# Kernel tuning notes

Hardware: AMD Instinct MI355X
Metric: run time of the kernel (lower is better)

Reference implementation:

```python
import jax, jax.numpy as jnp
import numpy as np

K = 1024
DIM = 64
BETA = 0.25  # commitment coefficient


def setup_inputs() -> dict:
    key = jax.random.key(0)
    k1, k2 = jax.random.split(key)
    x = jax.random.normal(k1, (32, 64, 64, 64), dtype=jnp.float32)  # [b, d, h, w]
    lookup_table = jax.random.normal(k2, (K, DIM), dtype=jnp.float32)  # [k, dim]
    return {"x": x, "lookup_table": lookup_table}


def reference(x, lookup_table):
    b, d, h, w = x.shape
    sg = jax.lax.stop_gradient
    # flatten to tokens: [b*h*w, dim]
    xf = jnp.transpose(x, (0, 2, 3, 1)).reshape(-1, d)
    # squared Euclidean distances (argmin-equivalent to cdist): [N, K]
    d2 = (jnp.sum(xf * xf, axis=1, keepdims=True)
          - 2.0 * (xf @ lookup_table.T)
          + jnp.sum(lookup_table * lookup_table, axis=1))
    q_x = jnp.argmin(d2, axis=1)  # [N]
    # gather codes and restore [b, d, h, w]
    x_e = jnp.transpose(lookup_table[q_x].reshape(b, h, w, d), (0, 3, 1, 2))
    # codebook + commitment loss (EMA update disabled in source)
    codebook_loss = jnp.mean((sg(x) - x_e) ** 2) + BETA * jnp.mean((x - sg(x_e)) ** 2)
    out = x + sg(x - x_e)
    return out, q_x.reshape(b, h, w), codebook_loss
```

## Files before the change

kernel.cpp:

```cpp
#include <hip/hip_runtime.h>

#define QX_OFF    8388608
#define LOSS_OFF  8519680
#define MARGIN_V  0.02f

typedef __attribute__((ext_vector_type(8))) short bf16x8;
typedef __attribute__((ext_vector_type(4))) float f32x4;
typedef unsigned long long u64;
typedef unsigned int u32;

static __device__ __forceinline__ unsigned short rne_bf16(float f) {
    unsigned u = __float_as_uint(f);
    u += 0x7FFFu + ((u >> 16) & 1u);
    return (unsigned short)(u >> 16);
}
static __device__ __forceinline__ float bf16_to_f(unsigned short h) {
    return __uint_as_float(((unsigned)h) << 16);
}
static __device__ __forceinline__ u64 pack4(unsigned short a, unsigned short b,
                                            unsigned short c, unsigned short d) {
    return (u64)a | ((u64)b << 16) | ((u64)c << 32) | ((u64)d << 48);
}

__global__ void vq_prep_kernel(const float* __restrict__ lut,
                               float* __restrict__ norms,
                               char* __restrict__ lutbfB,
                               int* __restrict__ flagcnt,
                               float* __restrict__ d_out) {
    int c = blockIdx.x * 256 + threadIdx.x;
    if (c == 0) { d_out[LOSS_OFF] = 0.f; *flagcnt = 0; }
    if (c < 1024) {
        const float4* c4 = reinterpret_cast<const float4*>(lut + c * 64);
        float s = 0.f;
        u64 hq[16], lq[16];
#pragma unroll
        for (int i = 0; i < 16; ++i) {
            float4 v = c4[i];
            s += v.x * v.x + v.y * v.y + v.z * v.z + v.w * v.w;
            unsigned short h0 = rne_bf16(v.x), h1 = rne_bf16(v.y),
                           h2 = rne_bf16(v.z), h3 = rne_bf16(v.w);
            unsigned short l0 = rne_bf16(v.x - bf16_to_f(h0)), l1 = rne_bf16(v.y - bf16_to_f(h1)),
                           l2 = rne_bf16(v.z - bf16_to_f(h2)), l3 = rne_bf16(v.w - bf16_to_f(h3));
            hq[i] = pack4(h0, h1, h2, h3);
            lq[i] = pack4(l0, l1, l2, l3);
        }
        norms[c] = s;
        u64* dst = reinterpret_cast<u64*>(lutbfB + c * 256);
#pragma unroll
        for (int i = 0; i < 16; ++i) { dst[i] = hq[i]; dst[16 + i] = lq[i]; }
    }
}

__launch_bounds__(512, 2)
__global__ void vq_screen_kernel(const float* __restrict__ x,
                                 const char* __restrict__ lutbfB,
                                 const float* __restrict__ norms,
                                 float* __restrict__ d_out,
                                 int* __restrict__ flaglist,
                                 int* __restrict__ flagcnt) {
    extern __shared__ char smc[];
    u32* sb = reinterpret_cast<u32*>(smc + 17408);

    const int tid  = threadIdx.x;
    const int w    = tid >> 6, lane = tid & 63;
    const int lcol = lane & 15, g = lane >> 4, g16 = g << 4;
    const int t0   = blockIdx.x * 512;
    const long xbase = (long)(t0 >> 12) * 262144 + (t0 & 4095);

    bf16x8 breg[8][4];
    float  cni[8];
#pragma unroll
    for (int ctl = 0; ctl < 8; ++ctl) {
        int c = (w * 8 + ctl) * 16 + lcol;
        const char* row = lutbfB + c * 256;
#pragma unroll
        for (int kb = 0; kb < 4; ++kb)
            breg[ctl][kb] = *reinterpret_cast<const bf16x8*>(row + kb * 64 + g16);
        cni[ctl] = 128.f + 0.5f * norms[c];
    }

    const int tok = tid & 15, qg = (tid >> 4) & 15, tl = tid >> 8;
    float xr[4];

#define LOADP(p) do {                                                          \
        const float* xp = x + xbase + (long)(4 * qg) * 4096                    \
                          + ((p) * 32 + tl * 16 + tok);                        \
        xr[0] = xp[0]; xr[1] = xp[4096]; xr[2] = xp[8192]; xr[3] = xp[12288];  \
    } while (0)

#define WRITEP(bufsel) do {                                                    \
        char* row = smc + (bufsel) * 8704 + tl * 4352 + tok * 272;             \
        unsigned short h0 = rne_bf16(xr[0]), h1 = rne_bf16(xr[1]),             \
                       h2 = rne_bf16(xr[2]), h3 = rne_bf16(xr[3]);             \
        unsigned short l0 = rne_bf16(xr[0] - bf16_to_f(h0)),                   \
                       l1 = rne_bf16(xr[1] - bf16_to_f(h1)),                   \
                       l2 = rne_bf16(xr[2] - bf16_to_f(h2)),                   \
                       l3 = rne_bf16(xr[3] - bf16_to_f(h3));                   \
        *reinterpret_cast<u64*>(row + qg * 8) =                                \
            pack4(h0, h1, h2, h3) ^ 0x8000800080008000ULL;                     \
        *reinterpret_cast<u64*>(row + 128 + qg * 8) =                          \
            pack4(l0, l1, l2, l3) ^ 0x8000800080008000ULL;                     \
    } while (0)

    LOADP(0); WRITEP(0); LOADP(1);

    const u32 VMASK = 0xFFFFFF80u;

    for (int tp = 0; tp < 16; ++tp) {
        if (tp < 15) WRITEP((tp + 1) & 1);
        if (tp < 14) LOADP(tp + 2);
        __syncthreads();
        const char* pbase = smc + (tp & 1) * 8704;

#pragma unroll
        for (int tl2 = 0; tl2 < 2; ++tl2) {
            const char* arow = pbase + tl2 * 4352 + lcol * 272;
            bf16x8 a0 = *reinterpret_cast<const bf16x8*>(arow + g16);
            bf16x8 a1 = *reinterpret_cast<const bf16x8*>(arow + 64 + g16);
            bf16x8 a2 = *reinterpret_cast<const bf16x8*>(arow + 128 + g16);
            bf16x8 a3 = *reinterpret_cast<const bf16x8*>(arow + 192 + g16);

            f32x4 acc[8];
#pragma unroll
            for (int ctl = 0; ctl < 8; ++ctl) {
                float v = cni[ctl];
                acc[ctl] = (f32x4){v, v, v, v};
            }
#pragma unroll
            for (int ctl = 0; ctl < 8; ++ctl)
                acc[ctl] = __builtin_amdgcn_mfma_f32_16x16x32_bf16(a0, breg[ctl][0], acc[ctl], 0, 0, 0);
#pragma unroll
            for (int ctl = 0; ctl < 8; ++ctl)
                acc[ctl] = __builtin_amdgcn_mfma_f32_16x16x32_bf16(a1, breg[ctl][1], acc[ctl], 0, 0, 0);
#pragma unroll
            for (int ctl = 0; ctl < 8; ++ctl)
                acc[ctl] = __builtin_amdgcn_mfma_f32_16x16x32_bf16(a0, breg[ctl][2], acc[ctl], 0, 0, 0);
#pragma unroll
            for (int ctl = 0; ctl < 8; ++ctl)
                acc[ctl] = __builtin_amdgcn_mfma_f32_16x16x32_bf16(a1, breg[ctl][3], acc[ctl], 0, 0, 0);
#pragma unroll
            for (int ctl = 0; ctl < 8; ++ctl)
                acc[ctl] = __builtin_amdgcn_mfma_f32_16x16x32_bf16(a2, breg[ctl][0], acc[ctl], 0, 0, 0);
#pragma unroll
            for (int ctl = 0; ctl < 8; ++ctl)
                acc[ctl] = __builtin_amdgcn_mfma_f32_16x16x32_bf16(a3, breg[ctl][1], acc[ctl], 0, 0, 0);

            u32 m1[4] = {0xFFFFFFFFu, 0xFFFFFFFFu, 0xFFFFFFFFu, 0xFFFFFFFFu};
            u32 m2[4] = {0xFFFFFFFFu, 0xFFFFFFFFu, 0xFFFFFFFFu, 0xFFFFFFFFu};
#pragma unroll
            for (int ctl = 0; ctl < 8; ++ctl) {
                u32 tag = (u32)((ctl << 4) | lcol);
#pragma unroll
                for (int r = 0; r < 4; ++r) {
                    u32 u = (__float_as_uint(acc[ctl][r]) & VMASK) | tag;
                    m2[r] = min(m2[r], max(m1[r], u));
                    m1[r] = min(m1[r], u);
                }
            }
#pragma unroll
            for (int m = 1; m <= 8; m <<= 1) {
#pragma unroll
                for (int r = 0; r < 4; ++r) {
                    u32 o1 = (u32)__shfl_xor((int)m1[r], m, 64);
                    u32 o2 = (u32)__shfl_xor((int)m2[r], m, 64);
                    m2[r] = min(min(m2[r], o2), max(m1[r], o1));
                    m1[r] = min(m1[r], o1);
                }
            }
            if (lcol == 0) {
#pragma unroll
                for (int r = 0; r < 4; ++r) {
                    int t = tp * 32 + tl2 * 16 + g * 4 + r;
                    sb[t * 17 + w * 2]     = m1[r];
                    sb[t * 17 + w * 2 + 1] = m2[r];
                }
            }
        }
        __syncthreads();
    }
#undef LOADP
#undef WRITEP

    {
        int t = tid;
        u32 b1 = sb[t * 17], b2 = sb[t * 17 + 1];
        int bw = 0;
#pragma unroll
        for (int ww = 1; ww < 8; ++ww) {
            u32 c1 = sb[t * 17 + ww * 2], c2 = sb[t * 17 + ww * 2 + 1];
            b2 = min(min(b2, c2), max(b1, c1));
            if (c1 < b1) { b1 = c1; bw = ww; }
        }
        int id = bw * 128 + (int)(b1 & 127u);
        d_out[QX_OFF + t0 + t] = (float)id;
        float gap = __uint_as_float(b2 & VMASK) - __uint_as_float(b1 & VMASK);
        if (gap <= MARGIN_V) {
            int slot = atomicAdd(flagcnt, 1);
            flaglist[slot] = t0 + t;
        }
    }
}

__global__ void vq_rescan_kernel(const float* __restrict__ x,
                                 const float* __restrict__ lut,
                                 const float* __restrict__ norms,
                                 float* __restrict__ d_out,
                                 const int* __restrict__ flaglist,
                                 const int* __restrict__ flagcnt) {
    __shared__ float xsh[4 * 68];
    const int tid = threadIdx.x, w = tid >> 6, lane = tid & 63;
    const int cnt = *flagcnt;
    const float4* lut4 = reinterpret_cast<const float4*>(lut);

    for (int idx = blockIdx.x * 4 + w; idx < cnt; idx += 2048 * 4) {
        int tk = flaglist[idx];
        xsh[w * 68 + lane] = x[(long)(tk >> 12) * 262144 + (tk & 4095) + (long)lane * 4096];
        const float4* xf4 = reinterpret_cast<const float4*>(xsh + w * 68);

        float acc[16];
#pragma unroll
        for (int k = 0; k < 16; ++k) acc[k] = 0.f;

        for (int q = 0; q < 16; ++q) {
            float4 xf = xf4[q];
#pragma unroll
            for (int k = 0; k < 16; ++k) {
                float4 cf = lut4[(lane + 64 * k) * 16 + q];
                acc[k] += xf.x * cf.x + xf.y * cf.y + xf.z * cf.z + xf.w * cf.w;
            }
        }
        float bv = 3.4e38f; int bj = 0;
#pragma unroll
        for (int k = 0; k < 16; ++k) {
            int j = lane + 64 * k;
            float v = norms[j] - 2.f * acc[k];
            if (v < bv) { bv = v; bj = j; }
        }
#pragma unroll
        for (int m = 1; m <= 32; m <<= 1) {
            float ov = __shfl_xor(bv, m, 64);
            int   oj = __shfl_xor(bj, m, 64);
            if (ov < bv || (ov == bv && oj < bj)) { bv = ov; bj = oj; }
        }
        if (lane == 0) d_out[QX_OFF + tk] = (float)bj;
    }
}

__global__ void vq_epilogue_kernel(const float* __restrict__ x,
                                   const float* __restrict__ lut,
                                   float* __restrict__ d_out) {
    __shared__ float cs[8192];
    __shared__ int qsh[128];
    const int tid = threadIdx.x;
    const int t0 = blockIdx.x * 128;
    const long xbase = (long)(t0 >> 12) * 262144 + (t0 & 4095);

    if (tid < 128) qsh[tid] = (int)d_out[QX_OFF + t0 + tid];
    __syncthreads();
    {
        int t = tid >> 1, half = tid & 1;
        int q = qsh[t];
        const float4* src = reinterpret_cast<const float4*>(lut + q * 64 + half * 32);
#pragma unroll
        for (int k = 0; k < 8; ++k) {
            float4 v = src[k];
            int dbase = half * 32 + k * 4;
            cs[(dbase + 0) * 128 + t] = v.x;
            cs[(dbase + 1) * 128 + t] = v.y;
            cs[(dbase + 2) * 128 + t] = v.z;
            cs[(dbase + 3) * 128 + t] = v.w;
        }
    }
    __syncthreads();

    float lsum = 0.f;
    {
        int t4 = (tid & 31) * 4, db = tid >> 5;
#pragma unroll
        for (int it = 0; it < 8; ++it) {
            int d = it * 8 + db;
            float4 xv = *reinterpret_cast<const float4*>(x + xbase + (long)d * 4096 + t4);
            float4 cv = *reinterpret_cast<const float4*>(cs + d * 128 + t4);
            float4 ov;
            ov.x = 2.f * xv.x - cv.x; ov.y = 2.f * xv.y - cv.y;
            ov.z = 2.f * xv.z - cv.z; ov.w = 2.f * xv.w - cv.w;
            *reinterpret_cast<float4*>(d_out + xbase + (long)d * 4096 + t4) = ov;
            float e0 = xv.x - cv.x, e1 = xv.y - cv.y, e2 = xv.z - cv.z, e3 = xv.w - cv.w;
            lsum += e0 * e0 + e1 * e1 + e2 * e2 + e3 * e3;
        }
    }
#pragma unroll
    for (int off = 32; off >= 1; off >>= 1)
        lsum += __shfl_down(lsum, off, 64);
    if ((tid & 63) == 0)
        atomicAdd(&d_out[LOSS_OFF], lsum * (1.25f / 8388608.f));
}

extern "C" void kernel_launch(void* const* d_in, const int* in_sizes, int n_in,
                              void* d_out, int out_size, void* d_ws, size_t ws_size,
                              hipStream_t stream) {
    const float* x   = (const float*)d_in[0];
    const float* lut = (const float*)d_in[1];
    float* out = (float*)d_out;
    char* ws = (char*)d_ws;
    float* norms    = (float*)ws;
    char*  lutbfB   = ws + 4096;
    int*   flagcnt  = (int*)(ws + 266240);
    int*   flaglist = (int*)(ws + 266256);

    vq_prep_kernel<<<4, 256, 0, stream>>>(lut, norms, lutbfB, flagcnt, out);
    vq_screen_kernel<<<256, 512, 52224, stream>>>(x, lutbfB, norms, out, flaglist, flagcnt);
    vq_rescan_kernel<<<2048, 256, 0, stream>>>(x, lut, norms, out, flaglist, flagcnt);
    vq_epilogue_kernel<<<1024, 256, 0, stream>>>(x, lut, out);
}
```

Before: 272.7 us.

## Halve tokens per screen block, aggregate flag atomics, replace loss atomics with reduction

The screen kernel now handles 256 tokens per block over 512 blocks instead of 512 over 256, which doubles the grid on a 256-CU device and trims shared memory. Flagged-token appends are aggregated per wavefront with a ballot and one atomic. The loss no longer uses per-wave float atomics; each epilogue block writes a partial sum and a small extra kernel reduces them, giving a deterministic result at the cost of one more launch. Each block reloads the codebook into registers, so halving tokens per block doubles that per-block overhead.

New measurement: 232.3 us. -14.8%, faster.

```diff
diff --git a/kernel.cpp b/kernel.cpp
--- a/kernel.cpp
+++ b/kernel.cpp
@@ -25,10 +25,9 @@
 __global__ void vq_prep_kernel(const float* __restrict__ lut,
                                float* __restrict__ norms,
                                char* __restrict__ lutbfB,
-                               int* __restrict__ flagcnt,
-                               float* __restrict__ d_out) {
+                               int* __restrict__ flagcnt) {
     int c = blockIdx.x * 256 + threadIdx.x;
-    if (c == 0) { d_out[LOSS_OFF] = 0.f; *flagcnt = 0; }
+    if (c == 0) *flagcnt = 0;
     if (c < 1024) {
         const float4* c4 = reinterpret_cast<const float4*>(lut + c * 64);
         float s = 0.f;
@@ -64,7 +63,7 @@
     const int tid  = threadIdx.x;
     const int w    = tid >> 6, lane = tid & 63;
     const int lcol = lane & 15, g = lane >> 4, g16 = g << 4;
-    const int t0   = blockIdx.x * 512;
+    const int t0   = blockIdx.x * 256;
     const long xbase = (long)(t0 >> 12) * 262144 + (t0 & 4095);
 
     bf16x8 breg[8][4];
@@ -106,9 +105,9 @@
 
     const u32 VMASK = 0xFFFFFF80u;
 
-    for (int tp = 0; tp < 16; ++tp) {
-        if (tp < 15) WRITEP((tp + 1) & 1);
-        if (tp < 14) LOADP(tp + 2);
+    for (int tp = 0; tp < 8; ++tp) {
+        if (tp < 7) WRITEP((tp + 1) & 1);
+        if (tp < 6) LOADP(tp + 2);
         __syncthreads();
         const char* pbase = smc + (tp & 1) * 8704;
 
@@ -181,7 +180,7 @@
 #undef LOADP
 #undef WRITEP
 
-    {
+    if (tid < 256) {
         int t = tid;
         u32 b1 = sb[t * 17], b2 = sb[t * 17 + 1];
         int bw = 0;
@@ -194,9 +193,16 @@
         int id = bw * 128 + (int)(b1 & 127u);
         d_out[QX_OFF + t0 + t] = (float)id;
         float gap = __uint_as_float(b2 & VMASK) - __uint_as_float(b1 & VMASK);
-        if (gap <= MARGIN_V) {
-            int slot = atomicAdd(flagcnt, 1);
-            flaglist[slot] = t0 + t;
+        bool flag = (gap <= MARGIN_V);
+        u64 mask = __ballot(flag);
+        if (mask) {
+            int base = 0;
+            if (lane == 0) base = atomicAdd(flagcnt, __popcll(mask));
+            base = __shfl(base, 0, 64);
+            if (flag) {
+                int off = __popcll(mask & ((1ULL << lane) - 1ULL));
+                flaglist[base + off] = t0 + t;
+            }
         }
     }
 }
@@ -248,9 +254,11 @@
 
 __global__ void vq_epilogue_kernel(const float* __restrict__ x,
                                    const float* __restrict__ lut,
-                                   float* __restrict__ d_out) {
+                                   float* __restrict__ d_out,
+                                   float* __restrict__ partials) {
     __shared__ float cs[8192];
     __shared__ int qsh[128];
+    __shared__ float wsum[4];
     const int tid = threadIdx.x;
     const int t0 = blockIdx.x * 128;
     const long xbase = (long)(t0 >> 12) * 262144 + (t0 & 4095);
@@ -292,8 +300,24 @@
 #pragma unroll
     for (int off = 32; off >= 1; off >>= 1)
         lsum += __shfl_down(lsum, off, 64);
-    if ((tid & 63) == 0)
-        atomicAdd(&d_out[LOSS_OFF], lsum * (1.25f / 8388608.f));
+    if ((tid & 63) == 0) wsum[tid >> 6] = lsum;
+    __syncthreads();
+    if (tid == 0)
+        partials[blockIdx.x] = wsum[0] + wsum[1] + wsum[2] + wsum[3];
+}
+
+__global__ void vq_loss_kernel(const float* __restrict__ partials,
+                               float* __restrict__ d_out) {
+    __shared__ float wsum[4];
+    const int tid = threadIdx.x;
+    float s = partials[tid] + partials[tid + 256] + partials[tid + 512] + partials[tid + 768];
+#pragma unroll
+    for (int off = 32; off >= 1; off >>= 1)
+        s += __shfl_down(s, off, 64);
+    if ((tid & 63) == 0) wsum[tid >> 6] = s;
+    __syncthreads();
+    if (tid == 0)
+        d_out[LOSS_OFF] = (wsum[0] + wsum[1] + wsum[2] + wsum[3]) * (1.25f / 8388608.f);
 }
 
 extern "C" void kernel_launch(void* const* d_in, const int* in_sizes, int n_in,
@@ -307,9 +331,11 @@
     char*  lutbfB   = ws + 4096;
     int*   flagcnt  = (int*)(ws + 266240);
     int*   flaglist = (int*)(ws + 266256);
-
-    vq_prep_kernel<<<4, 256, 0, stream>>>(lut, norms, lutbfB, flagcnt, out);
-    vq_screen_kernel<<<256, 512, 52224, stream>>>(x, lutbfB, norms, out, flaglist, flagcnt);
+    float* partials = (float*)(ws + 790544);
+
+    vq_prep_kernel<<<4, 256, 0, stream>>>(lut, norms, lutbfB, flagcnt);
+    vq_screen_kernel<<<512, 512, 34816, stream>>>(x, lutbfB, norms, out, flaglist, flagcnt);
     vq_rescan_kernel<<<2048, 256, 0, stream>>>(x, lut, norms, out, flaglist, flagcnt);
-    vq_epilogue_kernel<<<1024, 256, 0, stream>>>(x, lut, out);
-}
+    vq_epilogue_kernel<<<1024, 256, 0, stream>>>(x, lut, out, partials);
+    vq_loss_kernel<<<1, 256, 0, stream>>>(partials, out);
+}
```
